# Optimization experiments

Hardware: AMD Instinct MI355X
Metric: run time of the kernel (lower is better)

The kernel has to match this reference:

```python
import jax, jax.numpy as jnp
import numpy as np

B, S, DIN, D, H, L, DFF = 256, 100, 64, 256, 8, 6, 1024
DK = D // H
SCALE = float(np.sqrt(DK))

def _pe(s, d):
    pos = np.arange(s)[:, None].astype(np.float32)
    div = np.exp(np.arange(0, d, 2).astype(np.float32) * (-np.log(10000.0) / d))
    pe = np.zeros((s, d), np.float32)
    pe[:, 0::2] = np.sin(pos * div)
    pe[:, 1::2] = np.cos(pos * div)
    return jnp.asarray(pe)

PE = _pe(S, D)  # (S, D) sinusoidal positional encoding

def _ln(x, g, b, eps=1e-5):
    m = jnp.mean(x, -1, keepdims=True)
    v = jnp.mean((x - m) ** 2, -1, keepdims=True)
    return (x - m) * jax.lax.rsqrt(v + eps) * g + b

def setup_inputs() -> dict:
    ks = iter(jax.random.split(jax.random.key(0), 32))
    def w(*shape):
        return jax.random.normal(next(ks), shape, jnp.float32) * 0.02
    z = lambda *s: jnp.zeros(s, jnp.float32)
    o = lambda *s: jnp.ones(s, jnp.float32)
    return {
        'x': jax.random.normal(next(ks), (B, S, DIN), jnp.float32),
        'W_in': w(DIN, D), 'b_in': z(D),
        'Wq': w(L, D, D), 'bq': z(L, D),
        'Wk': w(L, D, D), 'bk': z(L, D),
        'Wv': w(L, D, D), 'bv': z(L, D),
        'Wo': w(L, D, D), 'bo': z(L, D),
        'g1': o(L, D), 'be1': z(L, D),
        'W1': w(L, D, DFF), 'b1': z(L, DFF),
        'W2': w(L, DFF, D), 'b2': z(L, D),
        'g2': o(L, D), 'be2': z(L, D),
        'lnf_g': o(D), 'lnf_b': z(D),
        'Wr1': w(D, 128), 'br1': z(128), 'Wr2': w(128, 3), 'br2': z(3),
        'Wa1': w(D, 128), 'ba1': z(128), 'Wa2': w(128, 64), 'ba2': z(64), 'Wa3': w(64, 1), 'ba3': z(1),
        'Wc1': w(D, 64), 'bc1': z(64), 'Wc2': w(64, 1), 'bc2': z(1),
        'Wv1': w(D, 64), 'bv1': z(64), 'Wv2': w(64, 1), 'bv2': z(1),
    }

def reference(x, W_in, b_in, Wq, bq, Wk, bk, Wv, bv, Wo, bo, g1, be1, W1, b1, W2, b2, g2, be2, lnf_g, lnf_b, Wr1, br1, Wr2, br2, Wa1, ba1, Wa2, ba2, Wa3, ba3, Wc1, bc1, Wc2, bc2, Wv1, bv1, Wv2, bv2):
    h = x @ W_in + b_in + PE  # (B, S, D); dropout is identity in eval mode

    def block(h, p):
        wq, bq_, wk, bk_, wv, bv_, wo, bo_, g1_, be1_, w1, b1_, w2, b2_, g2_, be2_ = p
        q = (h @ wq + bq_).reshape(B, S, H, DK)
        k = (h @ wk + bk_).reshape(B, S, H, DK)
        v = (h @ wv + bv_).reshape(B, S, H, DK)
        s = jnp.einsum('bqhd,bkhd->bhqk', q, k) / SCALE
        a = jax.nn.softmax(s, axis=-1)
        o = jnp.einsum('bhqk,bkhd->bqhd', a, v).reshape(B, S, D)
        h = _ln(h + o @ wo + bo_, g1_, be1_)
        f = jax.nn.relu(h @ w1 + b1_) @ w2 + b2_
        h = _ln(h + f, g2_, be2_)
        return h, None

    h, _ = jax.lax.scan(block, h, (Wq, bq, Wk, bk, Wv, bv, Wo, bo, g1, be1, W1, b1, W2, b2, g2, be2))
    h = _ln(h, lnf_g, lnf_b)
    hf = h[:, -1]  # seq_lengths=None -> last token
    regime = jax.nn.softmax(jax.nn.relu(hf @ Wr1 + br1) @ Wr2 + br2, axis=-1)
    action = jnp.tanh(jax.nn.relu(jax.nn.relu(hf @ Wa1 + ba1) @ Wa2 + ba2) @ Wa3 + ba3)
    confidence = jax.nn.sigmoid(jax.nn.relu(hf @ Wc1 + bc1) @ Wc2 + bc2)
    volatility = jax.nn.relu(jax.nn.relu(hf @ Wv1 + bv1) @ Wv2 + bv2)
    return action, regime, confidence, volatility, hf
```

## Files before the change

### kernel.cpp

```cpp
#include <hip/hip_runtime.h>
#include <hip/hip_bf16.h>

#define BB   256
#define SS   100
#define DIN  64
#define DD   256
#define HH   8
#define LL   6
#define DFF  1024
#define MM   (BB*SS)
#define INV_SCALE 0.17677669529663687f

typedef unsigned short u16;
typedef __attribute__((__ext_vector_type__(8))) __bf16 bf16x8;
typedef __attribute__((__ext_vector_type__(8))) unsigned short u16x8;
typedef __attribute__((__ext_vector_type__(4))) float  f32x4;

__device__ __forceinline__ u16 f2bf(float f) {
    unsigned u = __float_as_uint(f);
    u += 0x7FFFu + ((u >> 16) & 1u);
    return (u16)(u >> 16);
}

#define MFMA16(a,b,c) __builtin_amdgcn_mfma_f32_16x16x32_bf16((a),(b),(c),0,0,0)

#if defined(__has_builtin)
#if __has_builtin(__builtin_amdgcn_global_load_lds)
#define HAVE_GLDS 1
#endif
#endif

#ifdef HAVE_GLDS
typedef __attribute__((address_space(1))) const void gas_void;
typedef __attribute__((address_space(3))) void las_void;
__device__ __forceinline__ void gload16(const u16* g, u16* l) {
    __builtin_amdgcn_global_load_lds((gas_void*)g, (las_void*)l, 16, 0, 0);
}
#else
__device__ __forceinline__ void gload16(const u16* g, u16* l) {
    const int lane = threadIdx.x & 63;
    *(uint4*)((char*)l + lane * 16) = *(const uint4*)g;
}
#endif

__global__ void pe_init_kernel(float* __restrict__ pe) {
    int i = blockIdx.x * blockDim.x + threadIdx.x;
    if (i >= SS * DD) return;
    int s = i >> 8;
    int c = i & 255;
    int ce = c & ~1;
    double div = exp((double)ce * -0.03597789207803197);
    double ang = (double)s * div;
    pe[i] = (float)((c & 1) ? cos(ang) : sin(ang));
}

__global__ void conv_bf16(const float* __restrict__ in, u16* __restrict__ out, int n) {
    int i = blockIdx.x * 256 + threadIdx.x;
    if (i < n) out[i] = f2bf(in[i]);
}

__global__ __launch_bounds__(256)
void transpose_conv(const float* __restrict__ in, u16* __restrict__ out,
                    int K, int N, long outLstride) {
    __shared__ float tile[32][33];
    const int k0 = blockIdx.x * 32, n0 = blockIdx.y * 32, lz = blockIdx.z;
    const int tx = threadIdx.x & 31, ty = threadIdx.x >> 5;
    const float* src = in + (size_t)lz * K * N;
#pragma unroll
    for (int i = 0; i < 4; ++i)
        tile[ty + i*8][tx] = src[(size_t)(k0 + ty + i*8) * N + n0 + tx];
    __syncthreads();
    u16* dst = out + (size_t)lz * outLstride;
#pragma unroll
    for (int i = 0; i < 4; ++i)
        dst[(size_t)(n0 + ty + i*8) * K + k0 + tx] = f2bf(tile[tx][ty + i*8]);
}

__global__ void pack_bias(const float* __restrict__ bq, const float* __restrict__ bk,
                          const float* __restrict__ bv, float* __restrict__ bqkv) {
    int idx = blockIdx.x * 256 + threadIdx.x;
    if (idx >= LL * 768) return;
    int l = idx / 768, c = idx % 768;
    float v = (c < 256) ? bq[l*256 + c] : (c < 512) ? bk[l*256 + c - 256] : bv[l*256 + c - 512];
    bqkv[idx] = v;
}

__global__ void pack_wh1(const float* __restrict__ Wr1, const float* __restrict__ Wa1,
                         const float* __restrict__ Wc1, const float* __restrict__ Wv1,
                         const float* __restrict__ br1, const float* __restrict__ ba1,
                         const float* __restrict__ bc1, const float* __restrict__ bv1,
                         u16* __restrict__ Wh1T, float* __restrict__ bh1) {
    int i = blockIdx.x * 256 + threadIdx.x;
    if (i < 384 * 256) {
        int n = i >> 8, k = i & 255;
        float v = (n < 128) ? Wr1[k*128 + n]
                : (n < 256) ? Wa1[k*128 + (n-128)]
                : (n < 320) ? Wc1[k*64  + (n-256)]
                            : Wv1[k*64  + (n-320)];
        Wh1T[(size_t)n * 256 + k] = f2bf(v);
    }
    if (i < 384) {
        float v = (i < 128) ? br1[i] : (i < 256) ? ba1[i-128]
                : (i < 320) ? bc1[i-256] : bv1[i-320];
        bh1[i] = v;
    }
}

template<int EPI, bool OF32, bool OBF16>
__global__ __launch_bounds__(256)
void mfma_gemm(const u16* __restrict__ A, const u16* __restrict__ Wt,
               const float* __restrict__ bias, const float* __restrict__ pe,
               float* __restrict__ Cf, u16* __restrict__ Cb,
               int M, int N, int K) {
    __shared__ u16 As[128 * 32];
    __shared__ u16 Bs[128 * 32];
    const int t = threadIdx.x, w = t >> 6, l = t & 63;
    const int bm = blockIdx.x * 128, bn = blockIdx.y * 128;
    const int wr = (w >> 1) * 64, wc = (w & 1) * 64;
    const int lr = l & 15, lk = (l >> 4) * 8, lq = (l >> 4) * 4;
    const int srow = l >> 2, scol = (l & 3) * 8;

    f32x4 acc[4][4] = {};
    const u16* Ag = &A [(size_t)(bm + w * 32 + srow) * K + scol];
    const u16* Bg = &Wt[(size_t)(bn + w * 32 + srow) * K + scol];
    u16* Al = &As[(w * 32) * 32];
    u16* Bl = &Bs[(w * 32) * 32];

    for (int k0 = 0; k0 < K; k0 += 32) {
        gload16(Ag + k0,                  Al);
        gload16(Ag + k0 + (size_t)16 * K, Al + 16 * 32);
        gload16(Bg + k0,                  Bl);
        gload16(Bg + k0 + (size_t)16 * K, Bl + 16 * 32);
        __syncthreads();

        bf16x8 af[4], bfr[4];
#pragma unroll
        for (int m = 0; m < 4; ++m) af[m]  = *(const bf16x8*)&As[(wr + m*16 + lr) * 32 + lk];
#pragma unroll
        for (int n = 0; n < 4; ++n) bfr[n] = *(const bf16x8*)&Bs[(wc + n*16 + lr) * 32 + lk];
#pragma unroll
        for (int m = 0; m < 4; ++m)
#pragma unroll
            for (int n = 0; n < 4; ++n)
                acc[m][n] = MFMA16(af[m], bfr[n], acc[m][n]);
        __syncthreads();
    }

#pragma unroll
    for (int n = 0; n < 4; ++n) {
        const int col = bn + wc + n*16 + lr;
        const float bv = bias[col];
#pragma unroll
        for (int m = 0; m < 4; ++m) {
#pragma unroll
            for (int j = 0; j < 4; ++j) {
                const int row = bm + wr + m*16 + lq + j;
                float v = acc[m][n][j] + bv;
                if (EPI == 1) v = fmaxf(v, 0.f);
                if (EPI == 2) v += pe[(row % SS) * DD + col];
                if (OF32)  Cf[(size_t)row * N + col] = v;
                if (OBF16) Cb[(size_t)row * N + col] = f2bf(v);
            }
        }
    }
}

__global__ __launch_bounds__(512)
void gemm_ln(const u16* __restrict__ A, const u16* __restrict__ Wt,
             const float* __restrict__ bias, const float* __restrict__ g,
             const float* __restrict__ be, float* __restrict__ h,
             u16* __restrict__ hb, int K) {
    __shared__ u16 As[64 * 32];
    __shared__ u16 Bs[256 * 32];
    __shared__ float red[64][8];
    const int t = threadIdx.x, w = t >> 6, l = t & 63;
    const int bm = blockIdx.x * 64;
    const int wr = w >> 2, wc = w & 3;
    const int lr = l & 15, lk = (l >> 4) * 8, lq = (l >> 4) * 4;
    const int crow = l >> 2, ccol = (l & 3) * 8;

    const int c0 = (w < 4) ? 3*w : 12 + 2*(w - 4);
    const int nc = (w < 4) ? 3 : 2;

    f32x4 acc[2][4] = {};

    for (int k0 = 0; k0 < K; k0 += 32) {
        for (int ci = 0; ci < nc; ++ci) {
            const int c = c0 + ci;
            if (c < 4)
                gload16(&A [(size_t)(bm + c*16 + crow) * K + k0 + ccol], &As[c*16*32]);
            else
                gload16(&Wt[(size_t)((c-4)*16 + crow) * K + k0 + ccol], &Bs[(c-4)*16*32]);
        }
        __syncthreads();

        bf16x8 af[2], bf[4];
#pragma unroll
        for (int mf = 0; mf < 2; ++mf) af[mf] = *(const bf16x8*)&As[(wr*32 + mf*16 + lr) * 32 + lk];
#pragma unroll
        for (int n = 0; n < 4; ++n)    bf[n]  = *(const bf16x8*)&Bs[(wc*64 + n*16 + lr) * 32 + lk];
#pragma unroll
        for (int mf = 0; mf < 2; ++mf)
#pragma unroll
            for (int n = 0; n < 4; ++n)
                acc[mf][n] = MFMA16(af[mf], bf[n], acc[mf][n]);
        __syncthreads();
    }

    float bv[4], gv[4], bev[4];
#pragma unroll
    for (int n = 0; n < 4; ++n) {
        int col = wc*64 + n*16 + lr;
        bv[n] = bias[col]; gv[n] = g[col]; bev[n] = be[col];
    }
#pragma unroll
    for (int mf = 0; mf < 2; ++mf) {
#pragma unroll
        for (int j = 0; j < 4; ++j) {
            const int rloc = wr*32 + mf*16 + lq + j;
            const int row  = bm + rloc;
            float s1 = 0.f, s2 = 0.f;
#pragma unroll
            for (int n = 0; n < 4; ++n) {
                float v = acc[mf][n][j] + bv[n] + h[(size_t)row * DD + wc*64 + n*16 + lr];
                acc[mf][n][j] = v;
                s1 += v; s2 += v * v;
            }
            s1 += __shfl_xor(s1, 1); s2 += __shfl_xor(s2, 1);
            s1 += __shfl_xor(s1, 2); s2 += __shfl_xor(s2, 2);
            s1 += __shfl_xor(s1, 4); s2 += __shfl_xor(s2, 4);
            s1 += __shfl_xor(s1, 8); s2 += __shfl_xor(s2, 8);
            if (lr == 0) { red[rloc][wc*2] = s1; red[rloc][wc*2+1] = s2; }
        }
    }
    __syncthreads();
#pragma unroll
    for (int mf = 0; mf < 2; ++mf) {
#pragma unroll
        for (int j = 0; j < 4; ++j) {
            const int rloc = wr*32 + mf*16 + lq + j;
            const int row  = bm + rloc;
            float s1 = red[rloc][0] + red[rloc][2] + red[rloc][4] + red[rloc][6];
            float s2 = red[rloc][1] + red[rloc][3] + red[rloc][5] + red[rloc][7];
            float mean = s1 * (1.f/DD);
            float var  = s2 * (1.f/DD) - mean*mean;
            float rstd = rsqrtf(var + 1e-5f);
#pragma unroll
            for (int n = 0; n < 4; ++n) {
                int col = wc*64 + n*16 + lr;
                float y = (acc[mf][n][j] - mean) * rstd * gv[n] + bev[n];
                h [(size_t)row * DD + col] = y;
                hb[(size_t)row * DD + col] = f2bf(y);
            }
        }
    }
}

__global__ __launch_bounds__(256)
void attn_mfma(const u16* __restrict__ qkv, u16* __restrict__ ao) {
    const int b = blockIdx.x >> 3, hh = blockIdx.x & 7;
    const int t = threadIdx.x, w = t >> 6, l = t & 63;
    const int lr = l & 15, lk = (l >> 4) * 8, lq = (l >> 4) * 4;
    __shared__ u16 Vt[32 * 136];
    __shared__ u16 Ps[4][32 * 136];
    const size_t rbase = (size_t)b * SS * 768;
    const int qc = hh * 32, kc = 256 + hh * 32, vc = 512 + hh * 32;

    for (int u = t; u < 400; u += 256) {
        int s = u >> 2, dp = (u & 3) * 8;
        u16x8 vv = *(const u16x8*)&qkv[rbase + (size_t)s * 768 + vc + dp];
#pragma unroll
        for (int e = 0; e < 8; ++e) Vt[(dp + e) * 136 + s] = vv[e];
    }
    for (int i = t; i < 32 * 36; i += 256) {
        int d = i / 36, s2 = 100 + i % 36;
        Vt[d * 136 + s2] = 0;
    }

    u16x8 qz = {0,0,0,0,0,0,0,0};
    u16x8 qfr[2];
#pragma unroll
    for (int m = 0; m < 2; ++m) {
        int r = w * 32 + m * 16 + lr;
        qfr[m] = (r < SS) ? *(const u16x8*)&qkv[rbase + (size_t)r * 768 + qc + lk] : qz;
    }

    f32x4 sacc[2][7] = {};
#pragma unroll
    for (int n = 0; n < 7; ++n) {
        int r = n * 16 + lr;
        u16x8 kfr = (r < SS) ? *(const u16x8*)&qkv[rbase + (size_t)r * 768 + kc + lk] : qz;
#pragma unroll
        for (int m = 0; m < 2; ++m)
            sacc[m][n] = MFMA16(*(bf16x8*)&qfr[m], *(bf16x8*)&kfr, sacc[m][n]);
    }

#pragma unroll
    for (int m = 0; m < 2; ++m) {
#pragma unroll
        for (int j = 0; j < 4; ++j) {
            float mx = -1e30f;
#pragma unroll
            for (int n = 0; n < 7; ++n) {
                float s = sacc[m][n][j] * INV_SCALE;
                if (n == 6 && lr >= 4) s = -1e30f;
                sacc[m][n][j] = s;
                mx = fmaxf(mx, s);
            }
            mx = fmaxf(mx, __shfl_xor(mx, 1));
            mx = fmaxf(mx, __shfl_xor(mx, 2));
            mx = fmaxf(mx, __shfl_xor(mx, 4));
            mx = fmaxf(mx, __shfl_xor(mx, 8));
            float sum = 0.f;
#pragma unroll
            for (int n = 0; n < 7; ++n) {
                float p = expf(sacc[m][n][j] - mx);
                if (n == 6 && lr >= 4) p = 0.f;
                sacc[m][n][j] = p;
                sum += p;
            }
            sum += __shfl_xor(sum, 1);
            sum += __shfl_xor(sum, 2);
            sum += __shfl_xor(sum, 4);
            sum += __shfl_xor(sum, 8);
            float inv = 1.f / sum;
#pragma unroll
            for (int n = 0; n < 7; ++n) sacc[m][n][j] *= inv;
        }
    }

    u16* myP = &Ps[w][0];
    for (int i = l; i < 32 * 24; i += 64) {
        int r = i / 24, c2 = 112 + i % 24;
        myP[r * 136 + c2] = 0;
    }
#pragma unroll
    for (int m = 0; m < 2; ++m)
#pragma unroll
        for (int n = 0; n < 7; ++n)
#pragma unroll
            for (int j = 0; j < 4; ++j)
                myP[(m*16 + lq + j) * 136 + n*16 + lr] = f2bf(sacc[m][n][j]);

    __syncthreads();

    f32x4 oacc[2][2] = {};
#pragma unroll
    for (int ks = 0; ks < 4; ++ks) {
        bf16x8 pf[2], vf[2];
#pragma unroll
        for (int m = 0; m < 2; ++m) pf[m] = *(const bf16x8*)&myP[(m*16 + lr) * 136 + ks*32 + lk];
#pragma unroll
        for (int n = 0; n < 2; ++n) vf[n] = *(const bf16x8*)&Vt [(n*16 + lr) * 136 + ks*32 + lk];
#pragma unroll
        for (int m = 0; m < 2; ++m)
#pragma unroll
            for (int n = 0; n < 2; ++n)
                oacc[m][n] = MFMA16(pf[m], vf[n], oacc[m][n]);
    }
#pragma unroll
    for (int m = 0; m < 2; ++m)
#pragma unroll
        for (int j = 0; j < 4; ++j) {
            int s = w*32 + m*16 + lq + j;
            if (s < SS) {
#pragma unroll
                for (int n = 0; n < 2; ++n)
                    ao[((size_t)(b*SS + s)) * DD + hh*32 + n*16 + lr] = f2bf(oacc[m][n][j]);
            }
        }
}

__global__ __launch_bounds__(256)
void lastrow_ln(const float* __restrict__ h, const float* __restrict__ g,
                const float* __restrict__ be, float* __restrict__ out,
                u16* __restrict__ hfb) {
    const int b = blockIdx.x;
    const int c = threadIdx.x;
    const float* row = h + (size_t)(b * SS + SS - 1) * DD;
    float x = row[c];

    float s1 = x, s2 = x * x;
#pragma unroll
    for (int o = 32; o > 0; o >>= 1) {
        s1 += __shfl_down(s1, o);
        s2 += __shfl_down(s2, o);
    }
    __shared__ float w1[4], w2[4];
    __shared__ float mean_s, rstd_s;
    const int wid = c >> 6, lane = c & 63;
    if (lane == 0) { w1[wid] = s1; w2[wid] = s2; }
    __syncthreads();
    if (c == 0) {
        float t1 = w1[0] + w1[1] + w1[2] + w1[3];
        float t2 = w2[0] + w2[1] + w2[2] + w2[3];
        float m = t1 * (1.0f / DD);
        float v = t2 * (1.0f / DD) - m * m;
        mean_s = m;
        rstd_s = rsqrtf(v + 1e-5f);
    }
    __syncthreads();
    float y = (x - mean_s) * rstd_s * g[c] + be[c];
    out[1536 + b * DD + c] = y;
    hfb[b * DD + c] = f2bf(y);
}

__global__ __launch_bounds__(256)
void heads2_kernel(const float* __restrict__ t1f,
                   const float* __restrict__ Wr2, const float* __restrict__ br2,
                   const float* __restrict__ Wa2, const float* __restrict__ ba2,
                   const float* __restrict__ Wa3, const float* __restrict__ ba3,
                   const float* __restrict__ Wc2, const float* __restrict__ bc2,
                   const float* __restrict__ Wv2, const float* __restrict__ bv2,
                   float* __restrict__ out) {
    const int b = blockIdx.x, t = threadIdx.x;
    __shared__ float t1[384];
    __shared__ float a2[64];
    __shared__ float lg[3];
    for (int i = t; i < 384; i += 256) t1[i] = t1f[(size_t)b * 384 + i];
    __syncthreads();

    if (t < 64) {
        float acc = ba2[t];
        for (int k = 0; k < 128; ++k) acc = fmaf(t1[128 + k], Wa2[k * 64 + t], acc);
        a2[t] = fmaxf(acc, 0.f);
    } else if (t == 64) {
        float acc = bc2[0];
        for (int k = 0; k < 64; ++k) acc = fmaf(t1[256 + k], Wc2[k], acc);
        out[1024 + b] = 1.0f / (1.0f + expf(-acc));
    } else if (t == 65) {
        float acc = bv2[0];
        for (int k = 0; k < 64; ++k) acc = fmaf(t1[320 + k], Wv2[k], acc);
        out[1280 + b] = fmaxf(acc, 0.f);
    } else if (t >= 66 && t < 69) {
        int r = t - 66;
        float acc = br2[r];
        for (int k = 0; k < 128; ++k) acc = fmaf(t1[k], Wr2[k * 3 + r], acc);
        lg[r] = acc;
    }
    __syncthreads();
    if (t == 0) {
        float m = fmaxf(lg[0], fmaxf(lg[1], lg[2]));
        float e0 = expf(lg[0] - m), e1 = expf(lg[1] - m), e2 = expf(lg[2] - m);
        float inv = 1.0f / (e0 + e1 + e2);
        out[256 + b * 3 + 0] = e0 * inv;
        out[256 + b * 3 + 1] = e1 * inv;
        out[256 + b * 3 + 2] = e2 * inv;
    }
    if (t < 64) {
        float p = a2[t] * Wa3[t];
        p += __shfl_xor(p, 1);
        p += __shfl_xor(p, 2);
        p += __shfl_xor(p, 4);
        p += __shfl_xor(p, 8);
        p += __shfl_xor(p, 16);
        p += __shfl_xor(p, 32);
        if (t == 0) out[b] = tanhf(p + ba3[0]);
    }
}

extern "C" void kernel_launch(void* const* d_in, const int* in_sizes, int n_in,
                              void* d_out, int out_size, void* d_ws, size_t ws_size,
                              hipStream_t stream) {
    const float* x    = (const float*)d_in[0];
    const float* W_in = (const float*)d_in[1];
    const float* b_in = (const float*)d_in[2];
    const float* Wq   = (const float*)d_in[3];
    const float* bq   = (const float*)d_in[4];
    const float* Wk   = (const float*)d_in[5];
    const float* bk   = (const float*)d_in[6];
    const float* Wv   = (const float*)d_in[7];
    const float* bv   = (const float*)d_in[8];
    const float* Wo   = (const float*)d_in[9];
    const float* bo   = (const float*)d_in[10];
    const float* g1   = (const float*)d_in[11];
    const float* be1  = (const float*)d_in[12];
    const float* W1   = (const float*)d_in[13];
    const float* b1   = (const float*)d_in[14];
    const float* W2   = (const float*)d_in[15];
    const float* b2   = (const float*)d_in[16];
    const float* g2   = (const float*)d_in[17];
    const float* be2  = (const float*)d_in[18];
    const float* lnf_g = (const float*)d_in[19];
    const float* lnf_b = (const float*)d_in[20];
    const float* Wr1  = (const float*)d_in[21];
    const float* br1  = (const float*)d_in[22];
    const float* Wr2  = (const float*)d_in[23];
    const float* br2  = (const float*)d_in[24];
    const float* Wa1  = (const float*)d_in[25];
    const float* ba1  = (const float*)d_in[26];
    const float* Wa2  = (const float*)d_in[27];
    const float* ba2  = (const float*)d_in[28];
    const float* Wa3  = (const float*)d_in[29];
    const float* ba3  = (const float*)d_in[30];
    const float* Wc1  = (const float*)d_in[31];
    const float* bc1  = (const float*)d_in[32];
    const float* Wc2  = (const float*)d_in[33];
    const float* bc2  = (const float*)d_in[34];
    const float* Wv1  = (const float*)d_in[35];
    const float* bv1  = (const float*)d_in[36];
    const float* Wv2  = (const float*)d_in[37];
    const float* bv2  = (const float*)d_in[38];
    float* out = (float*)d_out;

    char* w8 = (char*)d_ws;
    float* pe    = (float*)w8;  w8 += (size_t)SS * DD * 4;
    float* h     = (float*)w8;  w8 += (size_t)MM * DD * 4;
    u16*   hb    = (u16*)w8;    w8 += (size_t)MM * DD * 2;
    u16*   xb    = (u16*)w8;    w8 += (size_t)MM * DIN * 2;
    u16*   qkvb  = (u16*)w8;    w8 += (size_t)MM * 768 * 2;
    u16*   ao    = (u16*)w8;    w8 += (size_t)MM * DD * 2;
    u16*   ffn1b = (u16*)w8;    w8 += (size_t)MM * DFF * 2;
    u16*   WinT  = (u16*)w8;    w8 += (size_t)DIN * DD * 2;
    u16*   WqkvT = (u16*)w8;    w8 += (size_t)LL * 768 * DD * 2;
    u16*   WoT   = (u16*)w8;    w8 += (size_t)LL * DD * DD * 2;
    u16*   W1T   = (u16*)w8;    w8 += (size_t)LL * DFF * DD * 2;
    u16*   W2T   = (u16*)w8;    w8 += (size_t)LL * DD * DFF * 2;
    float* bqkv  = (float*)w8;  w8 += (size_t)LL * 768 * 4;
    u16*   Wh1T  = (u16*)w8;    w8 += (size_t)384 * 256 * 2;
    float* bh1   = (float*)w8;  w8 += (size_t)384 * 4;
    u16*   hfb   = (u16*)w8;    w8 += (size_t)BB * DD * 2;
    float* t1f   = (float*)w8;  w8 += (size_t)BB * 384 * 4;

    pe_init_kernel<<<(SS * DD + 255) / 256, 256, 0, stream>>>(pe);
    conv_bf16<<<(MM * DIN + 255) / 256, 256, 0, stream>>>(x, xb, MM * DIN);
    transpose_conv<<<dim3(DIN/32, DD/32, 1), 256, 0, stream>>>(W_in, WinT, DIN, DD, (long)DIN * DD);
    transpose_conv<<<dim3(8, 8, 6),  256, 0, stream>>>(Wq, WqkvT,             DD, DD, 768L * DD);
    transpose_conv<<<dim3(8, 8, 6),  256, 0, stream>>>(Wk, WqkvT + DD*DD,     DD, DD, 768L * DD);
    transpose_conv<<<dim3(8, 8, 6),  256, 0, stream>>>(Wv, WqkvT + 2*DD*DD,   DD, DD, 768L * DD);
    transpose_conv<<<dim3(8, 8, 6),  256, 0, stream>>>(Wo, WoT, DD, DD, (long)DD * DD);
    transpose_conv<<<dim3(8, 32, 6), 256, 0, stream>>>(W1, W1T, DD, DFF, (long)DD * DFF);
    transpose_conv<<<dim3(32, 8, 6), 256, 0, stream>>>(W2, W2T, DFF, DD, (long)DD * DFF);
    pack_bias<<<(LL * 768 + 255) / 256, 256, 0, stream>>>(bq, bk, bv, bqkv);
    pack_wh1<<<384, 256, 0, stream>>>(Wr1, Wa1, Wc1, Wv1, br1, ba1, bc1, bv1, Wh1T, bh1);

    mfma_gemm<2, true, true><<<dim3(MM/128, DD/128), 256, 0, stream>>>(
        xb, WinT, b_in, pe, h, hb, MM, DD, DIN);

    for (int l = 0; l < LL; ++l) {
        mfma_gemm<0, false, true><<<dim3(MM/128, 768/128), 256, 0, stream>>>(
            hb, WqkvT + (size_t)l*768*DD, bqkv + l*768, nullptr, nullptr, qkvb, MM, 768, DD);
        attn_mfma<<<BB * HH, 256, 0, stream>>>(qkvb, ao);
        gemm_ln<<<MM/64, 512, 0, stream>>>(
            ao, WoT + (size_t)l*DD*DD, bo + l*DD, g1 + l*DD, be1 + l*DD, h, hb, DD);
        mfma_gemm<1, false, true><<<dim3(MM/128, DFF/128), 256, 0, stream>>>(
            hb, W1T + (size_t)l*DFF*DD, b1 + l*DFF, nullptr, nullptr, ffn1b, MM, DFF, DD);
        gemm_ln<<<MM/64, 512, 0, stream>>>(
            ffn1b, W2T + (size_t)l*DD*DFF, b2 + l*DD, g2 + l*DD, be2 + l*DD, h, hb, DFF);
    }

    lastrow_ln<<<BB, 256, 0, stream>>>(h, lnf_g, lnf_b, out, hfb);

    mfma_gemm<1, true, false><<<dim3(2, 3), 256, 0, stream>>>(
        hfb, Wh1T, bh1, nullptr, t1f, nullptr, 256, 384, 256);

    heads2_kernel<<<BB, 256, 0, stream>>>(t1f,
        Wr2, br2, Wa2, ba2, Wa3, ba3, Wc2, bc2, Wv2, bv2, out);
}
```

Measured before the change: 952.3 us.

## Fuse FFN up-projection, ReLU, down-projection and LayerNorm into one kernel

Replaces the separate W1 GEMM and the W2 GEMM+LayerNorm kernels with a single kernel per 64-row tile. The kernel computes 128-column chunks of the ReLU hidden activation into shared memory and accumulates them straight into the W2 output, so the MM×1024 bf16 intermediate never goes to global memory. In exchange, the weight B-operands are read directly from global memory with no shared-memory staging, and each block redoes the full 1024-wide inner loop with only 400 blocks in flight. That may cost throughput compared with the tiled GEMM.

Result: slower. 1.271 ms (+33.5%).

```diff
diff --git a/kernel.cpp b/kernel.cpp
--- a/kernel.cpp
+++ b/kernel.cpp
@@ -249,6 +249,128 @@
             for (int n = 0; n < 4; ++n) {
                 int col = wc*64 + n*16 + lr;
                 float y = (acc[mf][n][j] - mean) * rstd * gv[n] + bev[n];
+                h [(size_t)row * DD + col] = y;
+                hb[(size_t)row * DD + col] = f2bf(y);
+            }
+        }
+    }
+}
+
+#define ASTR 264
+#define FSTR 136
+__global__ __launch_bounds__(512)
+void ffn_fused(const u16* __restrict__ Ain, const u16* __restrict__ W1t,
+               const u16* __restrict__ W2t, const float* __restrict__ b1,
+               const float* __restrict__ bias, const float* __restrict__ g,
+               const float* __restrict__ be, float* __restrict__ h,
+               u16* __restrict__ hb) {
+    __shared__ u16 As[64 * ASTR];
+    __shared__ u16 fc[64 * FSTR];
+    __shared__ float red[64][8];
+    const int t = threadIdx.x, w = t >> 6, l = t & 63;
+    const int bm = blockIdx.x * 64;
+    const int wr = w >> 2, wc = w & 3;
+    const int lr = l & 15, lk = (l >> 4) * 8, lq = (l >> 4) * 4;
+
+    for (int c = t; c < 64 * 32; c += 512) {
+        int row = c >> 5, part = c & 31;
+        *(uint4*)&As[row * ASTR + part * 8] =
+            *(const uint4*)&Ain[(size_t)(bm + row) * DD + part * 8];
+    }
+    __syncthreads();
+
+    f32x4 acc2[2][4] = {};
+
+    for (int kc = 0; kc < 8; ++kc) {
+        f32x4 fca[2][2] = {};
+#pragma unroll
+        for (int ks = 0; ks < 8; ++ks) {
+            bf16x8 a1[2], b1f[2];
+#pragma unroll
+            for (int mf = 0; mf < 2; ++mf)
+                a1[mf] = *(const bf16x8*)&As[(wr*32 + mf*16 + lr) * ASTR + ks*32 + lk];
+#pragma unroll
+            for (int nf = 0; nf < 2; ++nf)
+                b1f[nf] = *(const bf16x8*)&W1t[(size_t)(kc*128 + wc*32 + nf*16 + lr) * DD + ks*32 + lk];
+#pragma unroll
+            for (int mf = 0; mf < 2; ++mf)
+#pragma unroll
+                for (int nf = 0; nf < 2; ++nf)
+                    fca[mf][nf] = MFMA16(a1[mf], b1f[nf], fca[mf][nf]);
+        }
+        __syncthreads();
+#pragma unroll
+        for (int nf = 0; nf < 2; ++nf) {
+            const float bb = b1[kc*128 + wc*32 + nf*16 + lr];
+#pragma unroll
+            for (int mf = 0; mf < 2; ++mf)
+#pragma unroll
+                for (int j = 0; j < 4; ++j) {
+                    float v = fca[mf][nf][j] + bb;
+                    v = fmaxf(v, 0.f);
+                    fc[(wr*32 + mf*16 + lq + j) * FSTR + wc*32 + nf*16 + lr] = f2bf(v);
+                }
+        }
+        __syncthreads();
+#pragma unroll
+        for (int ks = 0; ks < 4; ++ks) {
+            bf16x8 a2[2], b2f[4];
+#pragma unroll
+            for (int mf = 0; mf < 2; ++mf)
+                a2[mf] = *(const bf16x8*)&fc[(wr*32 + mf*16 + lr) * FSTR + ks*32 + lk];
+#pragma unroll
+            for (int n = 0; n < 4; ++n)
+                b2f[n] = *(const bf16x8*)&W2t[(size_t)(wc*64 + n*16 + lr) * DFF + kc*128 + ks*32 + lk];
+#pragma unroll
+            for (int mf = 0; mf < 2; ++mf)
+#pragma unroll
+                for (int n = 0; n < 4; ++n)
+                    acc2[mf][n] = MFMA16(a2[mf], b2f[n], acc2[mf][n]);
+        }
+    }
+
+    float bv[4], gv[4], bev[4];
+#pragma unroll
+    for (int n = 0; n < 4; ++n) {
+        int col = wc*64 + n*16 + lr;
+        bv[n] = bias[col]; gv[n] = g[col]; bev[n] = be[col];
+    }
+#pragma unroll
+    for (int mf = 0; mf < 2; ++mf) {
+#pragma unroll
+        for (int j = 0; j < 4; ++j) {
+            const int rloc = wr*32 + mf*16 + lq + j;
+            const int row  = bm + rloc;
+            float s1 = 0.f, s2 = 0.f;
+#pragma unroll
+            for (int n = 0; n < 4; ++n) {
+                float v = acc2[mf][n][j] + bv[n] + h[(size_t)row * DD + wc*64 + n*16 + lr];
+                acc2[mf][n][j] = v;
+                s1 += v; s2 += v * v;
+            }
+            s1 += __shfl_xor(s1, 1); s2 += __shfl_xor(s2, 1);
+            s1 += __shfl_xor(s1, 2); s2 += __shfl_xor(s2, 2);
+            s1 += __shfl_xor(s1, 4); s2 += __shfl_xor(s2, 4);
+            s1 += __shfl_xor(s1, 8); s2 += __shfl_xor(s2, 8);
+            if (lr == 0) { red[rloc][wc*2] = s1; red[rloc][wc*2+1] = s2; }
+        }
+    }
+    __syncthreads();
+#pragma unroll
+    for (int mf = 0; mf < 2; ++mf) {
+#pragma unroll
+        for (int j = 0; j < 4; ++j) {
+            const int rloc = wr*32 + mf*16 + lq + j;
+            const int row  = bm + rloc;
+            float s1 = red[rloc][0] + red[rloc][2] + red[rloc][4] + red[rloc][6];
+            float s2 = red[rloc][1] + red[rloc][3] + red[rloc][5] + red[rloc][7];
+            float mean = s1 * (1.f/DD);
+            float var  = s2 * (1.f/DD) - mean*mean;
+            float rstd = rsqrtf(var + 1e-5f);
+#pragma unroll
+            for (int n = 0; n < 4; ++n) {
+                int col = wc*64 + n*16 + lr;
+                float y = (acc2[mf][n][j] - mean) * rstd * gv[n] + bev[n];
                 h [(size_t)row * DD + col] = y;
                 hb[(size_t)row * DD + col] = f2bf(y);
             }
@@ -510,7 +632,6 @@
     u16*   xb    = (u16*)w8;    w8 += (size_t)MM * DIN * 2;
     u16*   qkvb  = (u16*)w8;    w8 += (size_t)MM * 768 * 2;
     u16*   ao    = (u16*)w8;    w8 += (size_t)MM * DD * 2;
-    u16*   ffn1b = (u16*)w8;    w8 += (size_t)MM * DFF * 2;
     u16*   WinT  = (u16*)w8;    w8 += (size_t)DIN * DD * 2;
     u16*   WqkvT = (u16*)w8;    w8 += (size_t)LL * 768 * DD * 2;
     u16*   WoT   = (u16*)w8;    w8 += (size_t)LL * DD * DD * 2;
@@ -543,10 +664,9 @@
         attn_mfma<<<BB * HH, 256, 0, stream>>>(qkvb, ao);
         gemm_ln<<<MM/64, 512, 0, stream>>>(
             ao, WoT + (size_t)l*DD*DD, bo + l*DD, g1 + l*DD, be1 + l*DD, h, hb, DD);
-        mfma_gemm<1, false, true><<<dim3(MM/128, DFF/128), 256, 0, stream>>>(
-            hb, W1T + (size_t)l*DFF*DD, b1 + l*DFF, nullptr, nullptr, ffn1b, MM, DFF, DD);
-        gemm_ln<<<MM/64, 512, 0, stream>>>(
-            ffn1b, W2T + (size_t)l*DD*DFF, b2 + l*DD, g2 + l*DD, be2 + l*DD, h, hb, DFF);
+        ffn_fused<<<MM/64, 512, 0, stream>>>(
+            hb, W1T + (size_t)l*DFF*DD, W2T + (size_t)l*DD*DFF,
+            b1 + l*DFF, b2 + l*DD, g2 + l*DD, be2 + l*DD, h, hb);
     }
 
     lastrow_ln<<<BB, 256, 0, stream>>>(h, lnf_g, lnf_b, out, hfb);
```

## Double-buffer shared-memory tiles in the MFMA GEMM and GEMM+LayerNorm kernels

Applied to the files above, without the earlier changes.

Both GEMM kernels now use two shared-memory buffers per operand. The next K-slice is staged into the spare buffer before the MFMAs run on the current one, and one barrier per iteration replaces two. This is meant to overlap global-to-LDS loads with matrix math. The cost is double the LDS footprint, which may reduce occupancy. If gload16 is a synchronous load-and-store, the overlap depends on how the compiler schedules it.

Result: no change. 936.4 us (-1.7%).

```diff
diff --git a/kernel.cpp b/kernel.cpp
--- a/kernel.cpp
+++ b/kernel.cpp
@@ -112,8 +112,8 @@
                const float* __restrict__ bias, const float* __restrict__ pe,
                float* __restrict__ Cf, u16* __restrict__ Cb,
                int M, int N, int K) {
-    __shared__ u16 As[128 * 32];
-    __shared__ u16 Bs[128 * 32];
+    __shared__ u16 As[2][128 * 32];
+    __shared__ u16 Bs[2][128 * 32];
     const int t = threadIdx.x, w = t >> 6, l = t & 63;
     const int bm = blockIdx.x * 128, bn = blockIdx.y * 128;
     const int wr = (w >> 1) * 64, wc = (w & 1) * 64;
@@ -123,27 +123,34 @@
     f32x4 acc[4][4] = {};
     const u16* Ag = &A [(size_t)(bm + w * 32 + srow) * K + scol];
     const u16* Bg = &Wt[(size_t)(bn + w * 32 + srow) * K + scol];
-    u16* Al = &As[(w * 32) * 32];
-    u16* Bl = &Bs[(w * 32) * 32];
+
+    auto stage = [&](int buf, int k0) {
+        gload16(Ag + k0,                  &As[buf][(w * 32) * 32]);
+        gload16(Ag + k0 + (size_t)16 * K, &As[buf][(w * 32 + 16) * 32]);
+        gload16(Bg + k0,                  &Bs[buf][(w * 32) * 32]);
+        gload16(Bg + k0 + (size_t)16 * K, &Bs[buf][(w * 32 + 16) * 32]);
+    };
+
+    stage(0, 0);
+    __syncthreads();
+    int cur = 0;
 
     for (int k0 = 0; k0 < K; k0 += 32) {
-        gload16(Ag + k0,                  Al);
-        gload16(Ag + k0 + (size_t)16 * K, Al + 16 * 32);
-        gload16(Bg + k0,                  Bl);
-        gload16(Bg + k0 + (size_t)16 * K, Bl + 16 * 32);
-        __syncthreads();
+        if (k0 + 32 < K) stage(cur ^ 1, k0 + 32);
 
         bf16x8 af[4], bfr[4];
 #pragma unroll
-        for (int m = 0; m < 4; ++m) af[m]  = *(const bf16x8*)&As[(wr + m*16 + lr) * 32 + lk];
-#pragma unroll
-        for (int n = 0; n < 4; ++n) bfr[n] = *(const bf16x8*)&Bs[(wc + n*16 + lr) * 32 + lk];
+        for (int m = 0; m < 4; ++m) af[m]  = *(const bf16x8*)&As[cur][(wr + m*16 + lr) * 32 + lk];
+#pragma unroll
+        for (int n = 0; n < 4; ++n) bfr[n] = *(const bf16x8*)&Bs[cur][(wc + n*16 + lr) * 32 + lk];
 #pragma unroll
         for (int m = 0; m < 4; ++m)
 #pragma unroll
             for (int n = 0; n < 4; ++n)
                 acc[m][n] = MFMA16(af[m], bfr[n], acc[m][n]);
+
         __syncthreads();
+        cur ^= 1;
     }
 
 #pragma unroll
@@ -170,8 +177,8 @@
              const float* __restrict__ bias, const float* __restrict__ g,
              const float* __restrict__ be, float* __restrict__ h,
              u16* __restrict__ hb, int K) {
-    __shared__ u16 As[64 * 32];
-    __shared__ u16 Bs[256 * 32];
+    __shared__ u16 As[2][64 * 32];
+    __shared__ u16 Bs[2][256 * 32];
     __shared__ float red[64][8];
     const int t = threadIdx.x, w = t >> 6, l = t & 63;
     const int bm = blockIdx.x * 64;
@@ -184,27 +191,36 @@
 
     f32x4 acc[2][4] = {};
 
-    for (int k0 = 0; k0 < K; k0 += 32) {
+    auto stage = [&](int buf, int k0) {
         for (int ci = 0; ci < nc; ++ci) {
             const int c = c0 + ci;
             if (c < 4)
-                gload16(&A [(size_t)(bm + c*16 + crow) * K + k0 + ccol], &As[c*16*32]);
+                gload16(&A [(size_t)(bm + c*16 + crow) * K + k0 + ccol], &As[buf][c*16*32]);
             else
-                gload16(&Wt[(size_t)((c-4)*16 + crow) * K + k0 + ccol], &Bs[(c-4)*16*32]);
+                gload16(&Wt[(size_t)((c-4)*16 + crow) * K + k0 + ccol], &Bs[buf][(c-4)*16*32]);
         }
-        __syncthreads();
+    };
+
+    stage(0, 0);
+    __syncthreads();
+    int cur = 0;
+
+    for (int k0 = 0; k0 < K; k0 += 32) {
+        if (k0 + 32 < K) stage(cur ^ 1, k0 + 32);
 
         bf16x8 af[2], bf[4];
 #pragma unroll
-        for (int mf = 0; mf < 2; ++mf) af[mf] = *(const bf16x8*)&As[(wr*32 + mf*16 + lr) * 32 + lk];
-#pragma unroll
-        for (int n = 0; n < 4; ++n)    bf[n]  = *(const bf16x8*)&Bs[(wc*64 + n*16 + lr) * 32 + lk];
+        for (int mf = 0; mf < 2; ++mf) af[mf] = *(const bf16x8*)&As[cur][(wr*32 + mf*16 + lr) * 32 + lk];
+#pragma unroll
+        for (int n = 0; n < 4; ++n)    bf[n]  = *(const bf16x8*)&Bs[cur][(wc*64 + n*16 + lr) * 32 + lk];
 #pragma unroll
         for (int mf = 0; mf < 2; ++mf)
 #pragma unroll
             for (int n = 0; n < 4; ++n)
                 acc[mf][n] = MFMA16(af[mf], bf[n], acc[mf][n]);
+
         __syncthreads();
+        cur ^= 1;
     }
 
     float bv[4], gv[4], bev[4];
```
